# Performance work log

Hardware: AMD Instinct MI355X
Metric: run time of the kernel (lower is better)

## Reference

```python
import jax, jax.numpy as jnp
import numpy as np

INPUT_SIZE = 128
HID = 64
B, T = 256, 1024

def setup_inputs() -> dict:
    key = jax.random.key(0)
    ks = jax.random.split(key, 12)
    s1 = 1.0 / np.sqrt(HID)
    def u(k, shape):
        return jax.random.uniform(k, shape, jnp.float32, -s1, s1)
    return {
        "x": jax.random.normal(ks[0], (B, T, INPUT_SIZE), jnp.float32),
        "w_ih0": u(ks[1], (4 * HID, INPUT_SIZE)),
        "w_hh0": u(ks[2], (4 * HID, HID)),
        "b_ih0": u(ks[3], (4 * HID,)),
        "b_hh0": u(ks[4], (4 * HID,)),
        "w_ih1": u(ks[5], (4 * HID, HID)),
        "w_hh1": u(ks[6], (4 * HID, HID)),
        "b_ih1": u(ks[7], (4 * HID,)),
        "b_hh1": u(ks[8], (4 * HID,)),
        "w_out": u(ks[9], (1, HID)),
        "b_out": u(ks[10], (1,)),
    }

def _lstm(x, w_ih, w_hh, b_ih, b_hh):
    # x: [B, T, I] -> h sequence [B, T, H]; PyTorch gate order i, f, g, o
    Bb = x.shape[0]
    H = w_hh.shape[1]
    # precompute input contribution for all timesteps (one big GEMM)
    xg = jnp.einsum('bti,gi->btg', x, w_ih) + b_ih + b_hh  # [B, T, 4H]
    def step(carry, g_t):
        h, c = carry
        g = g_t + h @ w_hh.T  # [B, 4H]
        i, f, gg, o = jnp.split(g, 4, axis=-1)
        i = jax.nn.sigmoid(i)
        f = jax.nn.sigmoid(f)
        gg = jnp.tanh(gg)
        o = jax.nn.sigmoid(o)
        c = f * c + i * gg
        h = o * jnp.tanh(c)
        return (h, c), h
    init = (jnp.zeros((Bb, H), x.dtype), jnp.zeros((Bb, H), x.dtype))
    _, hs = jax.lax.scan(step, init, jnp.swapaxes(xg, 0, 1))  # [T, B, H]
    return jnp.swapaxes(hs, 0, 1)

def reference(x, w_ih0, w_hh0, b_ih0, b_hh0, w_ih1, w_hh1, b_ih1, b_hh1, w_out, b_out):
    h1 = _lstm(x, w_ih0, w_hh0, b_ih0, b_hh0)   # [B, T, H]
    h2 = _lstm(h1, w_ih1, w_hh1, b_ih1, b_hh1)  # [B, T, H]
    logits = jnp.einsum('bth,oh->bto', h2, w_out) + b_out  # [B, T, 1]
    return jax.nn.sigmoid(logits)
```

## Files before the change

kernel.cpp:

```cpp
#include <hip/hip_runtime.h>

#define BB 256
#define TT 1024
#define II 128
#define HH 64
#define BT (BB * TT)

typedef _Float16 h2 __attribute__((ext_vector_type(2)));
typedef _Float16 half8 __attribute__((ext_vector_type(8)));
typedef float f32x4 __attribute__((ext_vector_type(4)));
typedef unsigned int uint;
typedef unsigned short ushort;

#define DOT2(a, b, c) __builtin_amdgcn_fdot2((a), (b), (c), false)
#define BC(u) __builtin_bit_cast(h2, (uint)(u))
#define MFMA16(a, b, c) __builtin_amdgcn_mfma_f32_16x16x32_f16((a), (b), (c), 0, 0, 0)
#define SIG(v) __builtin_amdgcn_rcpf(1.0f + __expf(-(v)))
#define TNH(v) (1.0f - 2.0f * __builtin_amdgcn_rcpf(1.0f + __expf(2.0f * (v))))

#define BAR() asm volatile("s_waitcnt lgkmcnt(0)\n\ts_barrier" ::: "memory")

#define LDPK(P, ptr) uint P; { float2 _f = *(const float2*)(ptr); \
    h2 _h; _h[0] = (_Float16)_f.x; _h[1] = (_Float16)_f.y; \
    P = __builtin_bit_cast(uint, _h); }
#define PIN8(a,b,c,d,e,f,g,h_) asm volatile("" : "+v"(a),"+v"(b),"+v"(c),"+v"(d),"+v"(e),"+v"(f),"+v"(g),"+v"(h_));
#define LD8(P, base, o) \
    LDPK(P##0,(base)+(o)+ 0) LDPK(P##1,(base)+(o)+ 2) LDPK(P##2,(base)+(o)+ 4) LDPK(P##3,(base)+(o)+ 6) \
    LDPK(P##4,(base)+(o)+ 8) LDPK(P##5,(base)+(o)+10) LDPK(P##6,(base)+(o)+12) LDPK(P##7,(base)+(o)+14) \
    PIN8(P##0,P##1,P##2,P##3,P##4,P##5,P##6,P##7)

#define D8A(P, va, vb, c0, c1, c2, c3) \
    c0 = DOT2(BC(P##0), BC((va).x), c0); c1 = DOT2(BC(P##1), BC((va).y), c1); \
    c2 = DOT2(BC(P##2), BC((va).z), c2); c3 = DOT2(BC(P##3), BC((va).w), c3); \
    c0 = DOT2(BC(P##4), BC((vb).x), c0); c1 = DOT2(BC(P##5), BC((vb).y), c1); \
    c2 = DOT2(BC(P##6), BC((vb).z), c2); c3 = DOT2(BC(P##7), BC((vb).w), c3);

#define GDOT(G, s) { float a0=0.f,a1=0.f,a2=0.f,a3=0.f; \
    D8A(G##A, hv0, hv1, a0,a1,a2,a3) D8A(G##B, hv2, hv3, a0,a1,a2,a3) \
    D8A(G##C, hv4, hv5, a0,a1,a2,a3) D8A(G##D, hv6, hv7, a0,a1,a2,a3) \
    s = (a0 + a1) + (a2 + a3); }

#define LDHV(src) { const uint4* hq_ = (const uint4*)(src); \
    hv0=hq_[0]; hv1=hq_[1]; hv2=hq_[2]; hv3=hq_[3]; \
    hv4=hq_[4]; hv5=hq_[5]; hv6=hq_[6]; hv7=hq_[7]; }

__global__ __launch_bounds__(256)
void xg_mfma(const float* __restrict__ x, const float* __restrict__ w_ih0,
             ushort* __restrict__ xg)
{
    __shared__ __align__(16) _Float16 xt[64][136];
    __shared__ __align__(16) _Float16 wt[128][136];
    const int tid = threadIdx.x, lane = tid & 63, wv = tid >> 6;
    const int bt0 = blockIdx.x * 64;
    {
        const int row = tid >> 2, q = (tid & 3) * 32;
        const float4* src = (const float4*)(x + (size_t)(bt0 + row) * II + q);
        _Float16* dst = &xt[row][q];
        #pragma unroll
        for (int i = 0; i < 8; ++i) {
            float4 v = src[i];
            dst[4*i+0]=(_Float16)v.x; dst[4*i+1]=(_Float16)v.y;
            dst[4*i+2]=(_Float16)v.z; dst[4*i+3]=(_Float16)v.w;
        }
    }
    for (int nh = 0; nh < 2; ++nh) {
        __syncthreads();
        {
            const int n = tid >> 1, kh = (tid & 1) * 64;
            const int flatn = nh * 128 + n;
            const int srcrow = (flatn & 3) * 64 + (flatn >> 2);
            const float4* src = (const float4*)(w_ih0 + (size_t)srcrow * II + kh);
            _Float16* dst = &wt[n][kh];
            #pragma unroll
            for (int i = 0; i < 16; ++i) {
                float4 v = src[i];
                dst[4*i+0]=(_Float16)v.x; dst[4*i+1]=(_Float16)v.y;
                dst[4*i+2]=(_Float16)v.z; dst[4*i+3]=(_Float16)v.w;
            }
        }
        __syncthreads();
        const int m = wv * 16 + (lane & 15);
        const int kf = (lane >> 4) * 8;
        half8 a0 = *(const half8*)&xt[m][ 0 + kf];
        half8 a1 = *(const half8*)&xt[m][32 + kf];
        half8 a2 = *(const half8*)&xt[m][64 + kf];
        half8 a3 = *(const half8*)&xt[m][96 + kf];
        #pragma unroll
        for (int nt = 0; nt < 8; ++nt) {
            const int nloc = nt * 16 + (lane & 15);
            half8 b0 = *(const half8*)&wt[nloc][ 0 + kf];
            half8 b1 = *(const half8*)&wt[nloc][32 + kf];
            half8 b2 = *(const half8*)&wt[nloc][64 + kf];
            half8 b3 = *(const half8*)&wt[nloc][96 + kf];
            f32x4 acc = {0.f, 0.f, 0.f, 0.f};
            acc = MFMA16(a0, b0, acc); acc = MFMA16(a1, b1, acc);
            acc = MFMA16(a2, b2, acc); acc = MFMA16(a3, b3, acc);
            const int colg = nh * 128 + nt * 16 + (lane & 15);
            const int jj = colg >> 2, gg = colg & 3;
            const int r0 = wv * 16 + (lane >> 4) * 4;
            const int bloc = bt0 >> 10;
            const int tb = (bt0 & 1023) + r0;
            ushort* dst = xg + ((size_t)(bloc * 64 + jj) << 12) + gg;
            #pragma unroll
            for (int r = 0; r < 4; ++r) {
                _Float16 hv = (_Float16)acc[r];
                dst[(size_t)(tb + r) * 4] = __builtin_bit_cast(ushort, hv);
            }
        }
    }
}

__global__ __launch_bounds__(192) __attribute__((amdgpu_waves_per_eu(1, 1)))
void lstm2_core(const float* __restrict__ w_hh0,
                const float* __restrict__ b_ih0, const float* __restrict__ b_hh0,
                const float* __restrict__ w_ih1, const float* __restrict__ w_hh1,
                const float* __restrict__ b_ih1, const float* __restrict__ b_hh1,
                const ushort* __restrict__ xg, ushort* __restrict__ h1g)
{
    const int bb = blockIdx.x;
    const int w  = threadIdx.x >> 6;
    const int j  = threadIdx.x & 63;

    __shared__ __align__(16) uint  h0buf[8][32];
    __shared__ __align__(16) uint  h1buf[32];
    __shared__ __align__(16) float zbuf[8][64][4];

    const float* Wsel = (w == 0) ? w_hh0 : (w == 1) ? w_ih1 : w_hh1;
    const float* r0p = Wsel + (size_t)(  0 + j) * 64;
    const float* r1p = Wsel + (size_t)( 64 + j) * 64;
    const float* r2p = Wsel + (size_t)(128 + j) * 64;
    const float* r3p = Wsel + (size_t)(192 + j) * 64;
    LD8(G0A, r0p,  0) LD8(G0B, r0p, 16) LD8(G0C, r0p, 32) LD8(G0D, r0p, 48)
    LD8(G1A, r1p,  0) LD8(G1B, r1p, 16) LD8(G1C, r1p, 32) LD8(G1D, r1p, 48)
    LD8(G2A, r2p,  0) LD8(G2B, r2p, 16) LD8(G2C, r2p, 32) LD8(G2D, r2p, 48)
    LD8(G3A, r3p,  0) LD8(G3B, r3p, 16) LD8(G3C, r3p, 32) LD8(G3D, r3p, 48)

    float bI = 0.f, bF = 0.f, bG = 0.f, bO = 0.f;
    if (w == 0) {
        bI = b_ih0[j]       + b_hh0[j];
        bF = b_ih0[64 + j]  + b_hh0[64 + j];
        bG = b_ih0[128 + j] + b_hh0[128 + j];
        bO = b_ih0[192 + j] + b_hh0[192 + j];
    } else if (w == 2) {
        bI = b_ih1[j]       + b_hh1[j];
        bF = b_ih1[64 + j]  + b_hh1[64 + j];
        bG = b_ih1[128 + j] + b_hh1[128 + j];
        bO = b_ih1[192 + j] + b_hh1[192 + j];
    }

    float cst = 0.0f;
    const ushort* xb = xg + ((size_t)(bb * 64 + j) << 12);
    ushort* h1b = h1g + (size_t)bb * TT * 64 + j;

    uint4 hv0={0,0,0,0}, hv1={0,0,0,0}, hv2={0,0,0,0}, hv3={0,0,0,0};
    uint4 hv4={0,0,0,0}, hv5={0,0,0,0}, hv6={0,0,0,0}, hv7={0,0,0,0};
    f32x4 zr = {0.f, 0.f, 0.f, 0.f};
    uint4 q0 = {0,0,0,0}, q1 = {0,0,0,0};
    if (w == 0) {
        q0 = *(const uint4*)(xb);
        q1 = *(const uint4*)(xb + 8);
    }

#define PSTEP(KK, XLO, XHI) \
    if ((KK) < TT) { \
        float si, sf, sg, so; \
        GDOT(G0, si) GDOT(G1, sf) GDOT(G2, sg) GDOT(G3, so) \
        h2 xlo = BC(XLO), xhi = BC(XHI); \
        si += bI + (float)xlo[0]; sf += bF + (float)xlo[1]; \
        sg += bG + (float)xhi[0]; so += bO + (float)xhi[1]; \
        float ii = SIG(si), ff = SIG(sf), gg = TNH(sg), oo = SIG(so); \
        cst = fmaf(ff, cst, ii * gg); \
        float hval = oo * TNH(cst); \
        ((_Float16*)&h0buf[(KK) & 7][0])[j] = (_Float16)hval; \
        LDHV(&h0buf[(KK) & 7][0]); \
    }

#define Q1STEP(KK) { const int i_ = (KK); \
    if (i_ >= 3 && i_ < TT + 3) { \
        const int m_ = i_ - 3; \
        float si, sf, sg, so; \
        GDOT(G0, si) GDOT(G1, sf) GDOT(G2, sg) GDOT(G3, so) \
        f32x4 zv = {si, sf, sg, so}; \
        *(f32x4*)&zbuf[m_ & 7][j][0] = zv; \
    } \
    if (i_ >= 2 && i_ < TT + 2) LDHV(&h0buf[(i_ - 2) & 7][0]) }

#define Q2STEP(KK) { const int i_ = (KK); \
    if (i_ >= 6) { \
        const int m_ = i_ - 6; \
        float si, sf, sg, so; \
        GDOT(G0, si) GDOT(G1, sf) GDOT(G2, sg) GDOT(G3, so) \
        si += bI + zr[0]; sf += bF + zr[1]; \
        sg += bG + zr[2]; so += bO + zr[3]; \
        float ii = SIG(si), ff = SIG(sf), gg = TNH(sg), oo = SIG(so); \
        cst = fmaf(ff, cst, ii * gg); \
        float hval = oo * TNH(cst); \
        _Float16 hf = (_Float16)hval; \
        ((_Float16*)&h1buf[0])[j] = hf; \
        LDHV(&h1buf[0]); \
        h1b[(size_t)m_ * 64] = __builtin_bit_cast(ushort, hf); \
    } \
    if (i_ >= 5 && i_ < TT + 5) zr = *(const f32x4*)&zbuf[(i_ - 5) & 7][j][0]; }

    for (int k0 = 0; k0 < TT + 6; k0 += 2) {
        if (w == 0) {
            uint4 qn = q1;
            if (k0 + 4 < TT)
                qn = *(const uint4*)(xb + (size_t)(k0 + 4) * 4);
            PSTEP(k0,     q0.x, q0.y)
            PSTEP(k0 + 1, q0.z, q0.w)
            q0 = q1; q1 = qn;
        } else if (w == 1) {
            Q1STEP(k0)
            Q1STEP(k0 + 1)
        } else {
            Q2STEP(k0)
            Q2STEP(k0 + 1)
        }
        BAR();
    }
#undef PSTEP
#undef Q1STEP
#undef Q2STEP
}

__global__ __launch_bounds__(256)
void head_gemv(const ushort* __restrict__ h1g, const float* __restrict__ w_out,
               const float* __restrict__ b_out, float* __restrict__ outp)
{
    __shared__ float wsh[64];
    const int tid = threadIdx.x;
    if (tid < 64) wsh[tid] = w_out[tid];
    __syncthreads();
    const int bt = blockIdx.x * 256 + tid;
    const uint4* hp = (const uint4*)(h1g + (size_t)bt * 64);
    float s = 0.0f;
    #pragma unroll
    for (int i = 0; i < 8; ++i) {
        uint4 v = hp[i];
        const float* wp = &wsh[8 * i];
        h2 p;
        p = BC(v.x); s = fmaf((float)p[0], wp[0], s); s = fmaf((float)p[1], wp[1], s);
        p = BC(v.y); s = fmaf((float)p[0], wp[2], s); s = fmaf((float)p[1], wp[3], s);
        p = BC(v.z); s = fmaf((float)p[0], wp[4], s); s = fmaf((float)p[1], wp[5], s);
        p = BC(v.w); s = fmaf((float)p[0], wp[6], s); s = fmaf((float)p[1], wp[7], s);
    }
    outp[bt] = __builtin_amdgcn_rcpf(1.0f + __expf(-(s + b_out[0])));
}

extern "C" void kernel_launch(void* const* d_in, const int* in_sizes, int n_in,
                              void* d_out, int out_size, void* d_ws, size_t ws_size,
                              hipStream_t stream) {
    const float* x     = (const float*)d_in[0];
    const float* w_ih0 = (const float*)d_in[1];
    const float* w_hh0 = (const float*)d_in[2];
    const float* b_ih0 = (const float*)d_in[3];
    const float* b_hh0 = (const float*)d_in[4];
    const float* w_ih1 = (const float*)d_in[5];
    const float* w_hh1 = (const float*)d_in[6];
    const float* b_ih1 = (const float*)d_in[7];
    const float* b_hh1 = (const float*)d_in[8];
    const float* w_out = (const float*)d_in[9];
    const float* b_out = (const float*)d_in[10];
    float* out = (float*)d_out;

    ushort* xg  = (ushort*)d_ws;
    ushort* h1g = (ushort*)((char*)d_ws + (size_t)BT * 256 * 2);

    hipLaunchKernelGGL(xg_mfma, dim3(BT / 64), dim3(256), 0, stream, x, w_ih0, xg);
    hipLaunchKernelGGL(lstm2_core, dim3(BB), dim3(192), 0, stream,
                       w_hh0, b_ih0, b_hh0, w_ih1, w_hh1, b_ih1, b_hh1, xg, h1g);
    hipLaunchKernelGGL(head_gemv, dim3(BT / 256), dim3(256), 0, stream,
                       h1g, w_out, b_out, out);
}
```

Measured before the change: 811.3 us.

## Replace per-lane dot2 recurrent GEMV with MFMA 16x16x32 matrix ops

The recurrent h·W products in the fused two-layer LSTM core change from per-lane fdot2 chains to MFMA 16x16x32 f16 instructions, with weights repacked into the B-fragment layout held in registers. Each step issues 32 MFMAs per wave, and each lane then picks its four gate results out of the 16 accumulators. The goal is to shorten the per-timestep serial latency of the matvec on the critical path. The cost is that only one effective row of each MFMA is used, which wastes most of the matrix throughput and adds selection logic and MFMA latency that may outweigh the savings.

```diff
diff --git a/kernel.cpp b/kernel.cpp
--- a/kernel.cpp
+++ b/kernel.cpp
@@ -12,7 +12,6 @@
 typedef unsigned int uint;
 typedef unsigned short ushort;
 
-#define DOT2(a, b, c) __builtin_amdgcn_fdot2((a), (b), (c), false)
 #define BC(u) __builtin_bit_cast(h2, (uint)(u))
 #define MFMA16(a, b, c) __builtin_amdgcn_mfma_f32_16x16x32_f16((a), (b), (c), 0, 0, 0)
 #define SIG(v) __builtin_amdgcn_rcpf(1.0f + __expf(-(v)))
@@ -20,29 +19,10 @@
 
 #define BAR() asm volatile("s_waitcnt lgkmcnt(0)\n\ts_barrier" ::: "memory")
 
-#define LDPK(P, ptr) uint P; { float2 _f = *(const float2*)(ptr); \
-    h2 _h; _h[0] = (_Float16)_f.x; _h[1] = (_Float16)_f.y; \
-    P = __builtin_bit_cast(uint, _h); }
-#define PIN8(a,b,c,d,e,f,g,h_) asm volatile("" : "+v"(a),"+v"(b),"+v"(c),"+v"(d),"+v"(e),"+v"(f),"+v"(g),"+v"(h_));
-#define LD8(P, base, o) \
-    LDPK(P##0,(base)+(o)+ 0) LDPK(P##1,(base)+(o)+ 2) LDPK(P##2,(base)+(o)+ 4) LDPK(P##3,(base)+(o)+ 6) \
-    LDPK(P##4,(base)+(o)+ 8) LDPK(P##5,(base)+(o)+10) LDPK(P##6,(base)+(o)+12) LDPK(P##7,(base)+(o)+14) \
-    PIN8(P##0,P##1,P##2,P##3,P##4,P##5,P##6,P##7)
-
-#define D8A(P, va, vb, c0, c1, c2, c3) \
-    c0 = DOT2(BC(P##0), BC((va).x), c0); c1 = DOT2(BC(P##1), BC((va).y), c1); \
-    c2 = DOT2(BC(P##2), BC((va).z), c2); c3 = DOT2(BC(P##3), BC((va).w), c3); \
-    c0 = DOT2(BC(P##4), BC((vb).x), c0); c1 = DOT2(BC(P##5), BC((vb).y), c1); \
-    c2 = DOT2(BC(P##6), BC((vb).z), c2); c3 = DOT2(BC(P##7), BC((vb).w), c3);
-
-#define GDOT(G, s) { float a0=0.f,a1=0.f,a2=0.f,a3=0.f; \
-    D8A(G##A, hv0, hv1, a0,a1,a2,a3) D8A(G##B, hv2, hv3, a0,a1,a2,a3) \
-    D8A(G##C, hv4, hv5, a0,a1,a2,a3) D8A(G##D, hv6, hv7, a0,a1,a2,a3) \
-    s = (a0 + a1) + (a2 + a3); }
-
-#define LDHV(src) { const uint4* hq_ = (const uint4*)(src); \
-    hv0=hq_[0]; hv1=hq_[1]; hv2=hq_[2]; hv3=hq_[3]; \
-    hv4=hq_[4]; hv5=hq_[5]; hv6=hq_[6]; hv7=hq_[7]; }
+__device__ __forceinline__ uint pk2(float a, float b) {
+    h2 h; h[0] = (_Float16)a; h[1] = (_Float16)b;
+    return __builtin_bit_cast(uint, h);
+}
 
 __global__ __launch_bounds__(256)
 void xg_mfma(const float* __restrict__ x, const float* __restrict__ w_ih0,
@@ -120,20 +100,27 @@
     const int bb = blockIdx.x;
     const int w  = threadIdx.x >> 6;
     const int j  = threadIdx.x & 63;
+    const int qq = j >> 4, cc = j & 15;
 
     __shared__ __align__(16) uint  h0buf[8][32];
     __shared__ __align__(16) uint  h1buf[32];
     __shared__ __align__(16) float zbuf[8][64][4];
 
     const float* Wsel = (w == 0) ? w_hh0 : (w == 1) ? w_ih1 : w_hh1;
-    const float* r0p = Wsel + (size_t)(  0 + j) * 64;
-    const float* r1p = Wsel + (size_t)( 64 + j) * 64;
-    const float* r2p = Wsel + (size_t)(128 + j) * 64;
-    const float* r3p = Wsel + (size_t)(192 + j) * 64;
-    LD8(G0A, r0p,  0) LD8(G0B, r0p, 16) LD8(G0C, r0p, 32) LD8(G0D, r0p, 48)
-    LD8(G1A, r1p,  0) LD8(G1B, r1p, 16) LD8(G1C, r1p, 32) LD8(G1D, r1p, 48)
-    LD8(G2A, r2p,  0) LD8(G2B, r2p, 16) LD8(G2C, r2p, 32) LD8(G2D, r2p, 48)
-    LD8(G3A, r3p,  0) LD8(G3B, r3p, 16) LD8(G3C, r3p, 32) LD8(G3D, r3p, 48)
+    uint4 Bf[16][2];
+    #pragma unroll
+    for (int t = 0; t < 16; ++t) {
+        const int row = (t & 3) * 64 + (t >> 2) * 16 + cc;
+        const float* rp = Wsel + (size_t)row * 64 + qq * 8;
+        #pragma unroll
+        for (int kh = 0; kh < 2; ++kh) {
+            const float* p = rp + kh * 32;
+            uint4 v;
+            v.x = pk2(p[0], p[1]); v.y = pk2(p[2], p[3]);
+            v.z = pk2(p[4], p[5]); v.w = pk2(p[6], p[7]);
+            Bf[t][kh] = v;
+        }
+    }
 
     float bI = 0.f, bF = 0.f, bG = 0.f, bO = 0.f;
     if (w == 0) {
@@ -152,8 +139,10 @@
     const ushort* xb = xg + ((size_t)(bb * 64 + j) << 12);
     ushort* h1b = h1g + (size_t)bb * TT * 64 + j;
 
-    uint4 hv0={0,0,0,0}, hv1={0,0,0,0}, hv2={0,0,0,0}, hv3={0,0,0,0};
-    uint4 hv4={0,0,0,0}, hv5={0,0,0,0}, hv6={0,0,0,0}, hv7={0,0,0,0};
+    const f32x4 ZR4 = {0.f, 0.f, 0.f, 0.f};
+    const int qlo = qq & 1, qhi = qq >> 1;
+
+    half8 af0 = {0,0,0,0,0,0,0,0}, af1 = {0,0,0,0,0,0,0,0};
     f32x4 zr = {0.f, 0.f, 0.f, 0.f};
     uint4 q0 = {0,0,0,0}, q1 = {0,0,0,0};
     if (w == 0) {
@@ -161,10 +150,26 @@
         q1 = *(const uint4*)(xb + 8);
     }
 
+#define LDAF(SRC) { const char* hb_ = (const char*)(SRC); \
+    af0 = *(const half8*)(hb_ + (qq << 4)); \
+    af1 = *(const half8*)(hb_ + 64 + (qq << 4)); }
+
+#define GEMV16(SI, SF, SG, SO) { \
+    f32x4 D[16]; \
+    _Pragma("unroll") \
+    for (int t = 0; t < 16; ++t) { \
+        f32x4 d_ = MFMA16(af0, __builtin_bit_cast(half8, Bf[t][0]), ZR4); \
+        D[t] = MFMA16(af1, __builtin_bit_cast(half8, Bf[t][1]), d_); } \
+    { float a_, b_; \
+      a_ = qlo ? D[ 4][0] : D[ 0][0]; b_ = qlo ? D[12][0] : D[ 8][0]; SI = qhi ? b_ : a_; \
+      a_ = qlo ? D[ 5][0] : D[ 1][0]; b_ = qlo ? D[13][0] : D[ 9][0]; SF = qhi ? b_ : a_; \
+      a_ = qlo ? D[ 6][0] : D[ 2][0]; b_ = qlo ? D[14][0] : D[10][0]; SG = qhi ? b_ : a_; \
+      a_ = qlo ? D[ 7][0] : D[ 3][0]; b_ = qlo ? D[15][0] : D[11][0]; SO = qhi ? b_ : a_; } }
+
 #define PSTEP(KK, XLO, XHI) \
     if ((KK) < TT) { \
         float si, sf, sg, so; \
-        GDOT(G0, si) GDOT(G1, sf) GDOT(G2, sg) GDOT(G3, so) \
+        GEMV16(si, sf, sg, so) \
         h2 xlo = BC(XLO), xhi = BC(XHI); \
         si += bI + (float)xlo[0]; sf += bF + (float)xlo[1]; \
         sg += bG + (float)xhi[0]; so += bO + (float)xhi[1]; \
@@ -172,24 +177,24 @@
         cst = fmaf(ff, cst, ii * gg); \
         float hval = oo * TNH(cst); \
         ((_Float16*)&h0buf[(KK) & 7][0])[j] = (_Float16)hval; \
-        LDHV(&h0buf[(KK) & 7][0]); \
+        LDAF(&h0buf[(KK) & 7][0]) \
     }
 
 #define Q1STEP(KK) { const int i_ = (KK); \
     if (i_ >= 3 && i_ < TT + 3) { \
         const int m_ = i_ - 3; \
         float si, sf, sg, so; \
-        GDOT(G0, si) GDOT(G1, sf) GDOT(G2, sg) GDOT(G3, so) \
+        GEMV16(si, sf, sg, so) \
         f32x4 zv = {si, sf, sg, so}; \
         *(f32x4*)&zbuf[m_ & 7][j][0] = zv; \
     } \
-    if (i_ >= 2 && i_ < TT + 2) LDHV(&h0buf[(i_ - 2) & 7][0]) }
+    if (i_ >= 2 && i_ < TT + 2) LDAF(&h0buf[(i_ - 2) & 7][0]) }
 
 #define Q2STEP(KK) { const int i_ = (KK); \
     if (i_ >= 6) { \
         const int m_ = i_ - 6; \
         float si, sf, sg, so; \
-        GDOT(G0, si) GDOT(G1, sf) GDOT(G2, sg) GDOT(G3, so) \
+        GEMV16(si, sf, sg, so) \
         si += bI + zr[0]; sf += bF + zr[1]; \
         sg += bG + zr[2]; so += bO + zr[3]; \
         float ii = SIG(si), ff = SIG(sf), gg = TNH(sg), oo = SIG(so); \
@@ -197,7 +202,7 @@
         float hval = oo * TNH(cst); \
         _Float16 hf = (_Float16)hval; \
         ((_Float16*)&h1buf[0])[j] = hf; \
-        LDHV(&h1buf[0]); \
+        LDAF(&h1buf[0]) \
         h1b[(size_t)m_ * 64] = __builtin_bit_cast(ushort, hf); \
     } \
     if (i_ >= 5 && i_ < TT + 5) zr = *(const f32x4*)&zbuf[(i_ - 5) & 7][j][0]; }
@@ -222,6 +227,8 @@
 #undef PSTEP
 #undef Q1STEP
 #undef Q2STEP
+#undef GEMV16
+#undef LDAF
 }
 
 __global__ __launch_bounds__(256)
```

After: 758.3 us. 1.07x faster.
